# Optimization experiments

Hardware: AMD Instinct MI355X
Metric: run time of the kernel (lower is better)

The kernel has to match this reference:

```python
import jax, jax.numpy as jnp
import numpy as np

B, T, D = 1, 2048, 1024
H, HD, NH = 16, 64, 2        # heads, head_dim, num_householder
EPS = 1e-5                   # RMSNorm eps
SCALE = HD ** -0.5           # query scale (k_dim**-0.5)


def setup_inputs() -> dict:
    key = jax.random.key(0)
    ks = jax.random.split(key, 10)
    init = lambda k, shape: jax.random.normal(k, shape, jnp.float32) * (shape[0] ** -0.5)
    return {
        "x": jax.random.normal(ks[0], (B, T, D), jnp.float32),
        "Wq": init(ks[1], (D, H * HD)),
        "Wk": init(ks[2], (D, NH * H * HD)),
        "Wv": init(ks[3], (D, NH * H * HD)),
        "Wb": init(ks[4], (D, NH * H)),
        "Wa": init(ks[5], (D, H)),
        "A_log": jnp.log(jax.random.uniform(ks[6], (H,), jnp.float32, 1e-2, 16.0)),
        "dt_bias": jnp.zeros((H,), jnp.float32),
        "Wg": init(ks[7], (D, H * HD)),
        "norm_weight": jnp.ones((HD,), jnp.float32),
        "Wo": init(ks[8], (H * HD, D)),
    }


def _l2norm(t):
    return t * jax.lax.rsqrt(jnp.sum(t * t, -1, keepdims=True) + 1e-6)


def _forward(x, Wq, Wk, Wv, Wb, Wa, A_log, dt_bias, Wg, norm_weight, Wo):
    # projections; householder sub-steps interleaved along time -> length T*NH
    q = _l2norm((x @ Wq).reshape(B, T, H, HD)) * SCALE            # [B,T,H,HD]
    k = _l2norm((x @ Wk).reshape(B, T, NH, H, HD)).reshape(B, T * NH, H, HD)
    v = (x @ Wv).reshape(B, T * NH, H, HD)
    # allow_neg_eigval=True -> beta in (0,2)
    beta = 2.0 * jax.nn.sigmoid((x @ Wb).reshape(B, T * NH, H))
    # gated decay applied once per token (first sub-step), zeros for the rest
    g = -jnp.exp(A_log) * jax.nn.softplus(x @ Wa + dt_bias)       # [B,T,H]
    g = jnp.concatenate(
        [g[:, :, None], jnp.zeros((B, T, NH - 1, H), g.dtype)], axis=2
    ).reshape(B, T * NH, H)
    qf = jnp.repeat(q, NH, axis=1)  # only sub-step NH-1 outputs are kept

    def step(S, inp):
        # S: [B,H,HD_k,HD_v] recurrent state
        k_t, v_t, b_t, g_t, q_t = inp
        S = S * jnp.exp(g_t)[..., None, None]
        pred = jnp.einsum('bhk,bhkv->bhv', k_t, S)
        dv = (v_t - pred) * b_t[..., None]
        S = S + k_t[..., None] * dv[..., None, :]
        o = jnp.einsum('bhk,bhkv->bhv', q_t, S)
        return S, o

    tm = lambda a: jnp.swapaxes(a, 0, 1)  # time-major for scan
    S0 = jnp.zeros((B, H, HD, HD), x.dtype)
    _, o = jax.lax.scan(step, S0, (tm(k), tm(v), tm(beta), tm(g), tm(qf)))
    o = tm(o[NH - 1::NH])  # last householder sub-step per token -> [B,T,H,HD]

    # gated RMSNorm (FusedRMSNormGated with swish gate)
    o = o * jax.lax.rsqrt(jnp.mean(o * o, -1, keepdims=True) + EPS) * norm_weight
    gate = (x @ Wg).reshape(B, T, H, HD)
    o = o * (gate * jax.nn.sigmoid(gate))
    return o.reshape(B, T, H * HD) @ Wo


def reference(x, Wq, Wk, Wv, Wb, Wa, A_log, dt_bias, Wg, norm_weight, Wo):
    return _forward(x, Wq, Wk, Wv, Wb, Wa, A_log, dt_bias, Wg, norm_weight, Wo)
```

## Files before the change

### kernel.cpp

```cpp
#include <hip/hip_runtime.h>
#include <stdint.h>


typedef unsigned short u16;
typedef __attribute__((ext_vector_type(8))) short bf16x8;
typedef __attribute__((ext_vector_type(4))) float f32x4;
typedef __attribute__((ext_vector_type(2))) float f32x2;
typedef __attribute__((ext_vector_type(4))) unsigned short u16x4;

#define TT 2048
#define NP 6208
#define NC 64
#define CS 64

__device__ __forceinline__ u16 f2bf(float f) {
  union { float f; uint32_t u; } v; v.f = f;
  uint32_t r = v.u + 0x7fffu + ((v.u >> 16) & 1u);
  return (u16)(r >> 16);
}
__device__ __forceinline__ float bf2f(u16 b) {
  union { uint32_t u; float f; } v; v.u = ((uint32_t)b) << 16; return v.f;
}

__device__ __forceinline__ void gload_lds16(const u16* g, u16* l) {
  __builtin_amdgcn_global_load_lds(
      (__attribute__((address_space(1))) const void*)(uintptr_t)g,
      (__attribute__((address_space(3))) void*)(uint32_t)(uintptr_t)l, 16, 0, 0);
}

__global__ void cvt_kernel(const float* __restrict__ src, u16* __restrict__ dst, long n) {
  long i = (long)blockIdx.x * 256 + threadIdx.x;
  if (i < n) dst[i] = f2bf(src[i]);
}

__global__ __launch_bounds__(256) void transAll_kernel(
    const float* __restrict__ Wq, const float* __restrict__ Wk,
    const float* __restrict__ Wv, const float* __restrict__ Wb,
    const float* __restrict__ Wa, const float* __restrict__ Wg,
    const float* __restrict__ Wo, u16* __restrict__ WT, u16* __restrict__ WoT) {
  int bx = blockIdx.x;
  const float* src; u16* dst; int cols;
  if      (bx < 32)  { src = Wq; dst = WT;                cols = 1024; }
  else if (bx < 96)  { src = Wk; dst = WT + 1024UL*1024;  cols = 2048; bx -= 32; }
  else if (bx < 160) { src = Wv; dst = WT + 3072UL*1024;  cols = 2048; bx -= 96; }
  else if (bx < 161) { src = Wb; dst = WT + 5120UL*1024;  cols = 32;   bx -= 160; }
  else if (bx < 162) { src = Wa; dst = WT + 5152UL*1024;  cols = 16;   bx -= 161; }
  else if (bx < 194) { src = Wg; dst = WT + 5168UL*1024;  cols = 1024; bx -= 162; }
  else               { src = Wo; dst = WoT;               cols = 1024; bx -= 194; }
  __shared__ float tile[32][33];
  const int tx = threadIdx.x & 31, ty = threadIdx.x >> 5;
  const int c0 = bx * 32, r0 = blockIdx.y * 32;
  for (int rr = ty; rr < 32; rr += 8)
    if (c0 + tx < cols) tile[rr][tx] = src[(size_t)(r0 + rr) * cols + c0 + tx];
  __syncthreads();
  for (int rr = ty; rr < 32; rr += 8)
    if (c0 + rr < cols) dst[(size_t)(c0 + rr) * 1024 + r0 + tx] = f2bf(tile[tx][rr]);
}

__global__ __launch_bounds__(256) void beacon_kernel(float* __restrict__ out, int n) {
  int i = blockIdx.x * 256 + threadIdx.x;
  if (i < n) out[i] = 4000.0f;
}

__global__ __launch_bounds__(256) void gemm128(const u16* __restrict__ A,
    const u16* __restrict__ BT, float* __restrict__ Cf, u16* __restrict__ Cb,
    int K, int lda, int ldc, int Nmax, int out_bf16) {
  const int bm = blockIdx.x * 128, bn = blockIdx.y * 128;
  const int tid = threadIdx.x, w = tid >> 6, lane = tid & 63;
  const int wr = (w >> 1) * 64, wc = (w & 1) * 64;
  const int quad = lane >> 4, r = lane & 15;
  __shared__ u16 As[128][32], Bs[128][32];
  f32x4 acc[4][4] = {};
  const int sr = w * 32 + (lane >> 2);
  const int sc = (lane & 3) * 8;
  const u16* gA0 = A  + (size_t)(bm + sr) * lda + sc;
  const u16* gA1 = A  + (size_t)(bm + sr + 16) * lda + sc;
  const u16* gB0 = BT + (size_t)(bn + sr) * K + sc;
  const u16* gB1 = BT + (size_t)(bn + sr + 16) * K + sc;
  u16* lA0 = &As[w * 32][0];
  u16* lA1 = &As[w * 32 + 16][0];
  u16* lB0 = &Bs[w * 32][0];
  u16* lB1 = &Bs[w * 32 + 16][0];
  for (int ks = 0; ks < K; ks += 32) {
    __syncthreads();
    gload_lds16(gA0 + ks, lA0);
    gload_lds16(gA1 + ks, lA1);
    gload_lds16(gB0 + ks, lB0);
    gload_lds16(gB1 + ks, lB1);
    __syncthreads();
    bf16x8 af[4], bf[4];
#pragma unroll
    for (int i = 0; i < 4; i++) af[i] = *(const bf16x8*)&As[wr + i * 16 + r][quad * 8];
#pragma unroll
    for (int j = 0; j < 4; j++) bf[j] = *(const bf16x8*)&Bs[wc + j * 16 + r][quad * 8];
#pragma unroll
    for (int i = 0; i < 4; i++)
#pragma unroll
      for (int j = 0; j < 4; j++)
        acc[i][j] = __builtin_amdgcn_mfma_f32_16x16x32_bf16(af[i], bf[j], acc[i][j], 0, 0, 0);
  }
#pragma unroll
  for (int i = 0; i < 4; i++)
#pragma unroll
    for (int j = 0; j < 4; j++)
#pragma unroll
      for (int rg = 0; rg < 4; rg++) {
        int row = bm + wr + i * 16 + quad * 4 + rg;
        int col = bn + wc + j * 16 + r;
        if (col < Nmax) {
          float v = acc[i][j][rg];
          if (out_bf16) Cb[(size_t)row * ldc + col] = f2bf(v);
          else          Cf[(size_t)row * ldc + col] = v;
        }
      }
}

__global__ __launch_bounds__(256) void prep_kernel(float* __restrict__ P,
    const float* __restrict__ A_log, const float* __restrict__ dt_bias,
    float* __restrict__ betab, float* __restrict__ gbuf) {
  const int t = blockIdx.x >> 2, w = threadIdx.x >> 6, lane = threadIdx.x & 63;
  const int h = (blockIdx.x & 3) * 4 + w;
  float* Pt = P + (size_t)t * NP;
  float qv = Pt[h * 64 + lane];
  float ss = qv * qv;
#pragma unroll
  for (int off = 32; off; off >>= 1) ss += __shfl_xor(ss, off);
  Pt[h * 64 + lane] = qv * rsqrtf(ss + 1e-6f) * 0.125f;
#pragma unroll
  for (int nh = 0; nh < 2; nh++) {
    float kv = Pt[1024 + nh * 1024 + h * 64 + lane];
    float ks = kv * kv;
#pragma unroll
    for (int off = 32; off; off >>= 1) ks += __shfl_xor(ks, off);
    Pt[1024 + nh * 1024 + h * 64 + lane] = kv * rsqrtf(ks + 1e-6f);
  }
  if (lane < 2) {
    float bb = Pt[5120 + lane * 16 + h];
    betab[(size_t)(2 * t + lane) * 16 + h] = 2.f / (1.f + expf(-bb));
  }
  if (lane == 0) {
    float a = Pt[5152 + h] + dt_bias[h];
    float sp = (a > 20.f) ? a : log1pf(expf(a));
    gbuf[t * 16 + h] = -expf(A_log[h]) * sp;
  }
}

__global__ __launch_bounds__(256, 1) void phaseA_kernel(const float* __restrict__ P,
    const float* __restrict__ betab, const float* __restrict__ gbuf,
    u16* __restrict__ Wbuf, u16* __restrict__ Uvbuf,
    float* __restrict__ Mbuf, float* __restrict__ NTbuf, float* __restrict__ cumbuf) {
  const int c = blockIdx.x, h = blockIdx.y, tid = threadIdx.x;
  const int bi = tid >> 4, bj = tid & 15;
  __shared__ float LA[64][68];
  __shared__ float LB[64][68];
  __shared__ float LC[64][68];
  __shared__ float cumch[64], betach[64], bbch[64], rowfl[64];
  const size_t base = ((size_t)c * 16 + h) * 4096;

  for (int e = tid; e < 4096; e += 256) {
    int i = e >> 6, d = e & 63, s = c * 64 + i, t = s >> 1, nh = s & 1;
    float kv = P[(size_t)t * NP + 1024 + nh * 1024 + h * 64 + d];
    LB[i][d] = kv; LA[d][i] = kv;
  }
  if (tid < 64) betach[tid] = betab[(size_t)(c * 64 + tid) * 16 + h];
  __syncthreads();
  if (tid == 0) {
    float cum = 0.f;
    for (int i = 0; i < 64; i++) {
      if ((i & 1) == 0) cum += gbuf[(c * 32 + (i >> 1)) * 16 + h];
      cumch[i] = cum;
    }
  }
  __syncthreads();
  if (tid < 64) {
    bbch[tid] = betach[tid] * expf(cumch[tid]);
    rowfl[tid] = expf(cumch[63] - cumch[tid]);
  }
  {
    float acc[4][4] = {};
#pragma unroll 4
    for (int d = 0; d < 64; d++) {
      f32x4 a = *(const f32x4*)&LA[d][4 * bi];
      f32x4 b = *(const f32x4*)&LA[d][4 * bj];
#pragma unroll
      for (int rr = 0; rr < 4; rr++)
#pragma unroll
        for (int cc = 0; cc < 4; cc++) acc[rr][cc] += a[rr] * b[cc];
    }
#pragma unroll
    for (int rr = 0; rr < 4; rr++)
#pragma unroll
      for (int cc = 0; cc < 4; cc++) {
        int i = 4 * bi + rr, j = 4 * bj + cc;
        LC[i][j] = (j < i) ? betach[i] * expf(cumch[i] - cumch[j]) * acc[rr][cc] : 0.f;
      }
  }
  __syncthreads();
  {
    int col = tid >> 2, part = tid & 3;
    if (part == 0) LA[col][0] = (col == 0) ? 1.f : 0.f;
    for (int i = 1; i < 64; i++) {
      float partial = 0.f;
      for (int j = col + part; j < i; j += 4) partial += LC[i][j] * LA[col][j];
      partial += __shfl_xor(partial, 1);
      partial += __shfl_xor(partial, 2);
      if (part == 0) LA[col][i] = ((i == col) ? 1.f : 0.f) - partial;
    }
  }
  __syncthreads();
  float vreg[16];
  {
    const int vi = tid >> 6, vd = tid & 63;
#pragma unroll
    for (int s = 0; s < 16; s++) {
      int i = vi + 4 * s, ss = c * 64 + i, t = ss >> 1, nh = ss & 1;
      vreg[s] = P[(size_t)t * NP + 3072 + nh * 1024 + h * 64 + vd];
    }
  }
  {
    float acc[4][4] = {};
#pragma unroll 4
    for (int j = 0; j < 4 * bi + 4; j++) {
      f32x4 tv = *(const f32x4*)&LA[j][4 * bi];
      f32x4 kv = *(const f32x4*)&LB[j][4 * bj];
      float bbj = bbch[j];
#pragma unroll
      for (int rr = 0; rr < 4; rr++)
#pragma unroll
        for (int cc = 0; cc < 4; cc++) acc[rr][cc] += tv[rr] * bbj * kv[cc];
    }
#pragma unroll
    for (int rr = 0; rr < 4; rr++) {
      int i = 4 * bi + rr;
      u16x4 wb;
#pragma unroll
      for (int cc = 0; cc < 4; cc++) { LC[i][4 * bj + cc] = acc[rr][cc]; wb[cc] = f2bf(acc[rr][cc]); }
      *(u16x4*)&Wbuf[base + (size_t)i * 64 + 4 * bj] = wb;
    }
  }
  __syncthreads();
  {
    const float bL = expf(cumch[63]);
    float acc[4][4] = {};
#pragma unroll 4
    for (int i = 0; i < 64; i++) {
      f32x4 kv = *(const f32x4*)&LB[i][4 * bi];
      f32x4 wv = *(const f32x4*)&LC[i][4 * bj];
      float rf = rowfl[i];
#pragma unroll
      for (int rr = 0; rr < 4; rr++)
#pragma unroll
        for (int cc = 0; cc < 4; cc++) acc[rr][cc] += rf * kv[rr] * wv[cc];
    }
#pragma unroll
    for (int rr = 0; rr < 4; rr++) {
      int m = 4 * bi + rr;
      f32x4 mv;
#pragma unroll
      for (int cc = 0; cc < 4; cc++)
        mv[cc] = ((m == 4 * bj + cc) ? bL : 0.f) - acc[rr][cc];
      *(f32x4*)&Mbuf[base + (size_t)m * 64 + 4 * bj] = mv;
    }
  }
  __syncthreads();
  {
    const int vi = tid >> 6, vd = tid & 63;
#pragma unroll
    for (int s = 0; s < 16; s++) LC[vi + 4 * s][vd] = vreg[s];
  }
  __syncthreads();
  float ua[4][4] = {};
  {
#pragma unroll 4
    for (int j = 0; j < 4 * bi + 4; j++) {
      f32x4 tv = *(const f32x4*)&LA[j][4 * bi];
      f32x4 vv = *(const f32x4*)&LC[j][4 * bj];
      float be = betach[j];
#pragma unroll
      for (int rr = 0; rr < 4; rr++)
#pragma unroll
        for (int cc = 0; cc < 4; cc++) ua[rr][cc] += tv[rr] * be * vv[cc];
    }
  }
  __syncthreads();
  {
#pragma unroll
    for (int rr = 0; rr < 4; rr++) {
      int i = 4 * bi + rr;
      u16x4 ub;
#pragma unroll
      for (int cc = 0; cc < 4; cc++) { LA[i][4 * bj + cc] = ua[rr][cc]; ub[cc] = f2bf(ua[rr][cc]); }
      *(u16x4*)&Uvbuf[base + (size_t)i * 64 + 4 * bj] = ub;
    }
  }
  __syncthreads();
  {
    float acc[4][4] = {};
#pragma unroll 4
    for (int i = 0; i < 64; i++) {
      f32x4 kv = *(const f32x4*)&LB[i][4 * bi];
      f32x4 uv = *(const f32x4*)&LA[i][4 * bj];
      float rf = rowfl[i];
#pragma unroll
      for (int rr = 0; rr < 4; rr++)
#pragma unroll
        for (int cc = 0; cc < 4; cc++) acc[rr][cc] += rf * kv[rr] * uv[cc];
    }
#pragma unroll
    for (int cc = 0; cc < 4; cc++) {
      f32x4 nv;
#pragma unroll
      for (int rr = 0; rr < 4; rr++) nv[rr] = acc[rr][cc];
      *(f32x4*)&NTbuf[base + (size_t)(4 * bj + cc) * 64 + 4 * bi] = nv;
    }
  }
  if (tid < 64) cumbuf[((size_t)c * 16 + h) * 64 + tid] = cumch[tid];
}

__global__ __launch_bounds__(64) void phaseB_kernel(const float* __restrict__ Mbuf,
    const float* __restrict__ NTbuf, u16* __restrict__ S0Tbuf) {
  const int g = blockIdx.x, h = blockIdx.y, l = threadIdx.x;
  const int c0 = 2 * g, c1 = 2 * g + 1;
  __shared__ float Ssh[2][2][64];
  Ssh[0][0][l] = 0.f; Ssh[0][1][l] = 0.f;
  float s0 = 0.f, s1 = 0.f;
  f32x4 mreg[16];
  float n0, n1;
  {
    const float* Mc = Mbuf + (size_t)h * 4096 + (size_t)l * 64;
#pragma unroll
    for (int q = 0; q < 16; q++) mreg[q] = *(const f32x4*)(Mc + 4 * q);
    const float* Nc = NTbuf + (size_t)h * 4096;
    n0 = Nc[c0 * 64 + l]; n1 = Nc[c1 * 64 + l];
  }
  __syncthreads();
  int p = 0;
  for (int c = 0; c < NC; c++) {
    const size_t base = ((size_t)c * 16 + h) * 4096;
    S0Tbuf[base + (size_t)c0 * 64 + l] = f2bf(s0);
    S0Tbuf[base + (size_t)c1 * 64 + l] = f2bf(s1);
    f32x4 mnext[16]; float nn0 = 0.f, nn1 = 0.f;
    if (c + 1 < NC) {
      const float* Mn = Mbuf + ((size_t)(c + 1) * 16 + h) * 4096 + (size_t)l * 64;
#pragma unroll
      for (int q = 0; q < 16; q++) mnext[q] = *(const f32x4*)(Mn + 4 * q);
      const float* Nn = NTbuf + ((size_t)(c + 1) * 16 + h) * 4096;
      nn0 = Nn[c0 * 64 + l]; nn1 = Nn[c1 * 64 + l];
    }
    float acc0 = n0, acc1 = n1;
#pragma unroll
    for (int q = 0; q < 16; q++) {
      f32x4 mv = mreg[q];
      f32x4 sv0 = *(const f32x4*)&Ssh[p][0][4 * q];
      f32x4 sv1 = *(const f32x4*)&Ssh[p][1][4 * q];
#pragma unroll
      for (int t = 0; t < 4; t++) { acc0 += mv[t] * sv0[t]; acc1 += mv[t] * sv1[t]; }
    }
    s0 = acc0; s1 = acc1;
    Ssh[p ^ 1][0][l] = s0; Ssh[p ^ 1][1][l] = s1;
    __syncthreads();
    p ^= 1;
#pragma unroll
    for (int q = 0; q < 16; q++) mreg[q] = mnext[q];
    n0 = nn0; n1 = nn1;
  }
}

__global__ __launch_bounds__(256) void phaseC_kernel(const float* __restrict__ P,
    const float* __restrict__ cumbuf, const u16* __restrict__ Wbuf,
    const u16* __restrict__ Uvbuf, const u16* __restrict__ S0Tbuf,
    const float* __restrict__ nw, u16* __restrict__ ybuf) {
  const int c = blockIdx.x, h = blockIdx.y, tid = threadIdx.x;
  const int rb = tid >> 4, jb = tid & 15;
  __shared__ float qT[64][36];
  __shared__ float kTc[64][68];
  __shared__ float Ul[64][68];
  __shared__ float PmT[64][36];
  __shared__ float cuml[64], nwl[64];
  const size_t base = (size_t)c * 16 + h;
  for (int e = tid; e < 2048; e += 256) {
    int r = e >> 6, d = e & 63;
    qT[d][r] = P[(size_t)(c * 32 + r) * NP + h * 64 + d];
  }
  for (int e = tid; e < 4096; e += 256) {
    int j = e >> 6, d = e & 63, s = c * 64 + j, t = s >> 1, nh = s & 1;
    kTc[d][j] = P[(size_t)t * NP + 1024 + nh * 1024 + h * 64 + d];
  }
  if (tid < 64) { cuml[tid] = cumbuf[base * 64 + tid]; nwl[tid] = nw[tid]; }
  __syncthreads();
  {
    float pa[2][4] = {};
#pragma unroll 4
    for (int d = 0; d < 64; d++) {
      f32x2 qv = *(const f32x2*)&qT[d][2 * rb];
      f32x4 kv = *(const f32x4*)&kTc[d][4 * jb];
#pragma unroll
      for (int rr = 0; rr < 2; rr++)
#pragma unroll
        for (int cc = 0; cc < 4; cc++) pa[rr][cc] += qv[rr] * kv[cc];
    }
#pragma unroll
    for (int rr = 0; rr < 2; rr++)
#pragma unroll
      for (int cc = 0; cc < 4; cc++) {
        int r = 2 * rb + rr, i = 2 * r + 1, j = 4 * jb + cc;
        PmT[j][r] = (j <= i) ? expf(cuml[i] - cuml[j]) * pa[rr][cc] : 0.f;
      }
  }
  __syncthreads();
  for (int e = tid; e < 4096; e += 256) {
    int i = e >> 6, m = e & 63;
    kTc[m][i] = bf2f(S0Tbuf[base * 4096 + e]);
    Ul[m][i]  = bf2f(Wbuf[base * 4096 + e]);
  }
  __syncthreads();
  float b2acc[4][4] = {};
  {
#pragma unroll 4
    for (int m = 0; m < 64; m++) {
      f32x4 wv = *(const f32x4*)&Ul[m][4 * rb];
      f32x4 sv = *(const f32x4*)&kTc[m][4 * jb];
#pragma unroll
      for (int rr = 0; rr < 4; rr++)
#pragma unroll
        for (int cc = 0; cc < 4; cc++) b2acc[rr][cc] += wv[rr] * sv[cc];
    }
  }
  __syncthreads();
#pragma unroll
  for (int rr = 0; rr < 4; rr++) {
    int i = 4 * rb + rr;
    u16x4 uv = *(const u16x4*)&Uvbuf[base * 4096 + (size_t)i * 64 + 4 * jb];
#pragma unroll
    for (int cc = 0; cc < 4; cc++)
      Ul[i][4 * jb + cc] = bf2f(f2bf(bf2f(uv[cc]) - b2acc[rr][cc]));
  }
  __syncthreads();
  float o[2][4];
  {
    float a1[2][4] = {}, a2[2][4] = {};
#pragma unroll 4
    for (int m = 0; m < 64; m++) {
      f32x2 qv = *(const f32x2*)&qT[m][2 * rb];
      f32x4 sv = *(const f32x4*)&kTc[m][4 * jb];
#pragma unroll
      for (int rr = 0; rr < 2; rr++)
#pragma unroll
        for (int cc = 0; cc < 4; cc++) a1[rr][cc] += qv[rr] * sv[cc];
    }
#pragma unroll 4
    for (int j = 0; j < 4 * rb + 4; j++) {
      f32x2 pv = *(const f32x2*)&PmT[j][2 * rb];
      f32x4 uv = *(const f32x4*)&Ul[j][4 * jb];
#pragma unroll
      for (int rr = 0; rr < 2; rr++)
#pragma unroll
        for (int cc = 0; cc < 4; cc++) a2[rr][cc] += pv[rr] * uv[cc];
    }
#pragma unroll
    for (int rr = 0; rr < 2; rr++) {
      float ec = expf(cuml[2 * (2 * rb + rr) + 1]);
#pragma unroll
      for (int cc = 0; cc < 4; cc++) o[rr][cc] = a1[rr][cc] * ec + a2[rr][cc];
    }
  }
  __syncthreads();
  float* ol = &qT[0][0];
#pragma unroll
  for (int rr = 0; rr < 2; rr++)
#pragma unroll
    for (int cc = 0; cc < 4; cc++)
      ol[(2 * rb + rr) * 68 + 4 * jb + cc] = o[rr][cc];
  __syncthreads();
  for (int e = tid; e < 2048; e += 256) {
    int r = e >> 6, d = e & 63;
    float ov = ol[r * 68 + d];
    float ss = ov * ov;
#pragma unroll
    for (int off = 32; off; off >>= 1) ss += __shfl_xor(ss, off);
    float on = ov * rsqrtf(ss * (1.f / 64.f) + 1e-5f) * nwl[d];
    int t = c * 32 + r;
    float gt = P[(size_t)t * NP + 5168 + h * 64 + d];
    float sw = gt / (1.f + expf(-gt));
    ybuf[(size_t)t * 1024 + h * 64 + d] = f2bf(on * sw);
  }
}

extern "C" void kernel_launch(void* const* d_in, const int* in_sizes, int n_in,
                              void* d_out, int out_size, void* d_ws, size_t ws_size,
                              hipStream_t stream) {
  const float* x       = (const float*)d_in[0];
  const float* Wq      = (const float*)d_in[1];
  const float* Wk      = (const float*)d_in[2];
  const float* Wv      = (const float*)d_in[3];
  const float* Wb      = (const float*)d_in[4];
  const float* Wa      = (const float*)d_in[5];
  const float* A_log   = (const float*)d_in[6];
  const float* dt_bias = (const float*)d_in[7];
  const float* Wg      = (const float*)d_in[8];
  const float* nw      = (const float*)d_in[9];
  const float* Wo      = (const float*)d_in[10];
  float* out = (float*)d_out;

  char* w = (char*)d_ws;
  size_t used = 0;
  auto alloc = [&](size_t bytes) {
    char* p = w + used; used += (bytes + 255) & ~(size_t)255; return p;
  };
  u16*   xb    = (u16*)  alloc(2048UL * 1024 * 2);
  u16*   WT    = (u16*)  alloc(6272UL * 1024 * 2);
  u16*   WoT   = (u16*)  alloc(1024UL * 1024 * 2);
  float* P     = (float*)alloc(2048UL * NP * 4);
  float* betab = (float*)alloc(4096UL * 16 * 4);
  float* gbuf  = (float*)alloc(2048UL * 16 * 4);
  u16*   ybuf  = (u16*)  alloc(2048UL * 1024 * 2);
  u16*   Wbuf  = (u16*)  alloc((size_t)NC * 16 * 4096 * 2);
  u16*   Uvbuf = (u16*)  alloc((size_t)NC * 16 * 4096 * 2);
  u16*   S0Tb  = (u16*)  alloc((size_t)NC * 16 * 4096 * 2);
  float* Mbuf  = (float*)alloc((size_t)NC * 16 * 4096 * 4);
  float* NTbuf = (float*)alloc((size_t)NC * 16 * 4096 * 4);
  float* cumb  = (float*)alloc((size_t)NC * 16 * 64 * 4);

  auto tgrid = [](long n) { return dim3((unsigned)((n + 255) / 256)); };
  if (used > ws_size) {
    beacon_kernel<<<tgrid(out_size), 256, 0, stream>>>(out, out_size);
    return;
  }

  hipMemsetAsync(WT + 6192UL * 1024, 0, 80UL * 1024 * 2, stream);

  cvt_kernel<<<tgrid(2048L*1024), 256, 0, stream>>>(x, xb, 2048L * 1024);
  transAll_kernel<<<dim3(226, 32), 256, 0, stream>>>(Wq, Wk, Wv, Wb, Wa, Wg, Wo, WT, WoT);

  gemm128<<<dim3(16, 49), 256, 0, stream>>>(xb, WT, P, nullptr, 1024, 1024, NP, NP, 0);
  prep_kernel<<<dim3(2048 * 4), 256, 0, stream>>>(P, A_log, dt_bias, betab, gbuf);

  phaseA_kernel<<<dim3(NC, 16), 256, 0, stream>>>(P, betab, gbuf, Wbuf, Uvbuf, Mbuf, NTbuf, cumb);
  phaseB_kernel<<<dim3(32, 16), 64, 0, stream>>>(Mbuf, NTbuf, S0Tb);
  phaseC_kernel<<<dim3(NC, 16), 256, 0, stream>>>(P, cumb, Wbuf, Uvbuf, S0Tb, nw, ybuf);

  gemm128<<<dim3(16, 8), 256, 0, stream>>>(ybuf, WoT, out, nullptr, 1024, 1024, 1024, 1024, 0);
}
```

Before: 420.2 us.

## Use bf16 MFMA for chunk Gram matrix and split state recurrence across waves

In phaseA, the key Gram matrix K·Kᵀ per chunk now comes from bf16 MFMA 16x16x32 instructions on a bf16 copy of keys in LDS, replacing scalar fp32 outer products. phaseB now uses two waves per block, each propagating one state column, and synchronises with wave barriers instead of block barriers. This shortens the serial per-chunk dependency chain. The cost is reduced precision in the Gram matrix that feeds the triangular solve.

```diff
diff --git a/kernel.cpp b/kernel.cpp
--- a/kernel.cpp
+++ b/kernel.cpp
@@ -154,13 +154,14 @@
   __shared__ float LA[64][68];
   __shared__ float LB[64][68];
   __shared__ float LC[64][68];
+  __shared__ u16 kb[64][72];
   __shared__ float cumch[64], betach[64], bbch[64], rowfl[64];
   const size_t base = ((size_t)c * 16 + h) * 4096;
 
   for (int e = tid; e < 4096; e += 256) {
     int i = e >> 6, d = e & 63, s = c * 64 + i, t = s >> 1, nh = s & 1;
     float kv = P[(size_t)t * NP + 1024 + nh * 1024 + h * 64 + d];
-    LB[i][d] = kv; LA[d][i] = kv;
+    LB[i][d] = kv; kb[i][d] = f2bf(kv);
   }
   if (tid < 64) betach[tid] = betab[(size_t)(c * 64 + tid) * 16 + h];
   __syncthreads();
@@ -177,23 +178,23 @@
     rowfl[tid] = expf(cumch[63] - cumch[tid]);
   }
   {
-    float acc[4][4] = {};
-#pragma unroll 4
-    for (int d = 0; d < 64; d++) {
-      f32x4 a = *(const f32x4*)&LA[d][4 * bi];
-      f32x4 b = *(const f32x4*)&LA[d][4 * bj];
-#pragma unroll
-      for (int rr = 0; rr < 4; rr++)
-#pragma unroll
-        for (int cc = 0; cc < 4; cc++) acc[rr][cc] += a[rr] * b[cc];
-    }
-#pragma unroll
-    for (int rr = 0; rr < 4; rr++)
-#pragma unroll
-      for (int cc = 0; cc < 4; cc++) {
-        int i = 4 * bi + rr, j = 4 * bj + cc;
-        LC[i][j] = (j < i) ? betach[i] * expf(cumch[i] - cumch[j]) * acc[rr][cc] : 0.f;
+    const int wv = tid >> 6, ln = tid & 63;
+    const int fr = ln & 15, qd = ln >> 4;
+    bf16x8 a0 = *(const bf16x8*)&kb[wv * 16 + fr][qd * 8];
+    bf16x8 a1 = *(const bf16x8*)&kb[wv * 16 + fr][qd * 8 + 32];
+#pragma unroll
+    for (int t = 0; t < 4; t++) {
+      bf16x8 b0 = *(const bf16x8*)&kb[t * 16 + fr][qd * 8];
+      bf16x8 b1 = *(const bf16x8*)&kb[t * 16 + fr][qd * 8 + 32];
+      f32x4 z = {0.f, 0.f, 0.f, 0.f};
+      z = __builtin_amdgcn_mfma_f32_16x16x32_bf16(a0, b0, z, 0, 0, 0);
+      z = __builtin_amdgcn_mfma_f32_16x16x32_bf16(a1, b1, z, 0, 0, 0);
+#pragma unroll
+      for (int rg = 0; rg < 4; rg++) {
+        int i = wv * 16 + qd * 4 + rg, j = t * 16 + fr;
+        LC[i][j] = (j < i) ? betach[i] * expf(cumch[i] - cumch[j]) * z[rg] : 0.f;
       }
+    }
   }
   __syncthreads();
   {
@@ -317,52 +318,49 @@
   if (tid < 64) cumbuf[((size_t)c * 16 + h) * 64 + tid] = cumch[tid];
 }
 
-__global__ __launch_bounds__(64) void phaseB_kernel(const float* __restrict__ Mbuf,
+__global__ __launch_bounds__(128) void phaseB_kernel(const float* __restrict__ Mbuf,
     const float* __restrict__ NTbuf, u16* __restrict__ S0Tbuf) {
-  const int g = blockIdx.x, h = blockIdx.y, l = threadIdx.x;
-  const int c0 = 2 * g, c1 = 2 * g + 1;
+  const int g = blockIdx.x, h = blockIdx.y;
+  const int wv = threadIdx.x >> 6, l = threadIdx.x & 63;
+  const int col = 2 * g + wv;
   __shared__ float Ssh[2][2][64];
-  Ssh[0][0][l] = 0.f; Ssh[0][1][l] = 0.f;
-  float s0 = 0.f, s1 = 0.f;
+  Ssh[0][wv][l] = 0.f;
+  float s = 0.f;
   f32x4 mreg[16];
-  float n0, n1;
+  float n;
   {
     const float* Mc = Mbuf + (size_t)h * 4096 + (size_t)l * 64;
 #pragma unroll
     for (int q = 0; q < 16; q++) mreg[q] = *(const f32x4*)(Mc + 4 * q);
-    const float* Nc = NTbuf + (size_t)h * 4096;
-    n0 = Nc[c0 * 64 + l]; n1 = Nc[c1 * 64 + l];
-  }
-  __syncthreads();
+    n = NTbuf[(size_t)h * 4096 + (size_t)col * 64 + l];
+  }
+  __builtin_amdgcn_wave_barrier();
   int p = 0;
   for (int c = 0; c < NC; c++) {
     const size_t base = ((size_t)c * 16 + h) * 4096;
-    S0Tbuf[base + (size_t)c0 * 64 + l] = f2bf(s0);
-    S0Tbuf[base + (size_t)c1 * 64 + l] = f2bf(s1);
-    f32x4 mnext[16]; float nn0 = 0.f, nn1 = 0.f;
+    S0Tbuf[base + (size_t)col * 64 + l] = f2bf(s);
+    f32x4 mnext[16]; float nn = 0.f;
     if (c + 1 < NC) {
       const float* Mn = Mbuf + ((size_t)(c + 1) * 16 + h) * 4096 + (size_t)l * 64;
 #pragma unroll
       for (int q = 0; q < 16; q++) mnext[q] = *(const f32x4*)(Mn + 4 * q);
-      const float* Nn = NTbuf + ((size_t)(c + 1) * 16 + h) * 4096;
-      nn0 = Nn[c0 * 64 + l]; nn1 = Nn[c1 * 64 + l];
-    }
-    float acc0 = n0, acc1 = n1;
+      nn = NTbuf[((size_t)(c + 1) * 16 + h) * 4096 + (size_t)col * 64 + l];
+    }
+    float acc = n;
 #pragma unroll
     for (int q = 0; q < 16; q++) {
       f32x4 mv = mreg[q];
-      f32x4 sv0 = *(const f32x4*)&Ssh[p][0][4 * q];
-      f32x4 sv1 = *(const f32x4*)&Ssh[p][1][4 * q];
-#pragma unroll
-      for (int t = 0; t < 4; t++) { acc0 += mv[t] * sv0[t]; acc1 += mv[t] * sv1[t]; }
-    }
-    s0 = acc0; s1 = acc1;
-    Ssh[p ^ 1][0][l] = s0; Ssh[p ^ 1][1][l] = s1;
-    __syncthreads();
+      f32x4 sv = *(const f32x4*)&Ssh[p][wv][4 * q];
+#pragma unroll
+      for (int t = 0; t < 4; t++) acc += mv[t] * sv[t];
+    }
+    s = acc;
+    Ssh[p ^ 1][wv][l] = s;
+    __builtin_amdgcn_wave_barrier();
     p ^= 1;
 #pragma unroll
     for (int q = 0; q < 16; q++) mreg[q] = mnext[q];
-    n0 = nn0; n1 = nn1;
+    n = nn;
   }
 }
 
@@ -536,7 +534,7 @@
   prep_kernel<<<dim3(2048 * 4), 256, 0, stream>>>(P, A_log, dt_bias, betab, gbuf);
 
   phaseA_kernel<<<dim3(NC, 16), 256, 0, stream>>>(P, betab, gbuf, Wbuf, Uvbuf, Mbuf, NTbuf, cumb);
-  phaseB_kernel<<<dim3(32, 16), 64, 0, stream>>>(Mbuf, NTbuf, S0Tb);
+  phaseB_kernel<<<dim3(32, 16), 128, 0, stream>>>(Mbuf, NTbuf, S0Tb);
   phaseC_kernel<<<dim3(NC, 16), 256, 0, stream>>>(P, cumb, Wbuf, Uvbuf, S0Tb, nw, ybuf);
 
   gemm128<<<dim3(16, 8), 256, 0, stream>>>(ybuf, WoT, out, nullptr, 1024, 1024, 1024, 1024, 0);
```

After: 484.6 us. +15.3%, slower.
